# Performance work log

Hardware: AMD Instinct MI355X
Metric: run time of the kernel (lower is better)

Reference implementation:

```python
import jax, jax.numpy as jnp
import numpy as np

H, D = 8, 16
HD = H * D
SCALE0 = float(1.0 / np.sqrt(D * 1))   # degree-0 dot-product scale (order m=1)
SCALE1 = float(1.0 / np.sqrt(D * 3))   # degree-1 dot-product scale (order m=3)
SHARED = float(np.sqrt(0.5))           # shared_scale = sqrt(1/2) for DOT_PROD + SHARED
NEG = -1e9


def _split_heads_q(x):  # (b,n,HD,m) -> (b,H,n,D,m)
    b, n, _, m = x.shape
    return x.reshape(b, n, H, D, m).transpose(0, 2, 1, 3, 4)


def _split_heads_k(x):  # (b,n,N,HD,m) -> (b,H,n,N,D,m)
    b, n, N, _, m = x.shape
    return x.reshape(b, n, N, H, D, m).transpose(0, 3, 1, 2, 4, 5)


def _augment_kv(k, v, feats, W_self, null_k, null_v):
    # attend_self: VNLinear self key/value; use_null_kv: learned null tokens.
    b, n = feats.shape[:2]
    m = feats.shape[-1]
    skv = jnp.einsum('oc,bncm->bnom', W_self, feats)          # (b,n,2HD,m)
    sk, sv = jnp.split(skv, 2, axis=-2)
    sk = _split_heads_q(sk)[:, :, :, None]                     # (b,H,n,1,D,m)
    sv = _split_heads_q(sv)[:, :, :, None]
    nk = jnp.broadcast_to(null_k[None, :, None, None], (b, H, n, 1, D, m))
    nv = jnp.broadcast_to(null_v[None, :, None, None], (b, H, n, 1, D, m))
    k = jnp.concatenate([nk, sk, k], axis=3)                   # (b,H,n,2+N,D,m)
    v = jnp.concatenate([nv, sv, v], axis=3)
    return k, v


def _merge_heads(x):  # (b,H,n,D,m) -> (b,n,HD,m)
    b, _, n, _, m = x.shape
    return x.transpose(0, 2, 1, 3, 4).reshape(b, n, HD, m)


def _forward(q0, k0, v0, q1, k1, v1, feats0, feats1, edges,
             W_self_kv0, W_self_kv1, W_bias, self_bias, null_bias,
             null_k0, null_v0, null_k1, null_v1, head_weights1,
             W_out0, W_out1, neighbor_mask):
    b, n, N = edges.shape[:3]
    q0h, k0h, v0h = _split_heads_q(q0), _split_heads_k(k0), _split_heads_k(v0)
    q1h, k1h, v1h = _split_heads_q(q1), _split_heads_k(k1), _split_heads_k(v1)
    k0h, v0h = _augment_kv(k0h, v0h, feats0, W_self_kv0, null_k0, null_v0)
    k1h, v1h = _augment_kv(k1h, v1h, feats1, W_self_kv1, null_k1, null_v1)

    # pair bias for degree 0 (to_order==1); prepend null/self bias columns
    edge_bias = jnp.einsum('bnje,he->bhnj', edges, W_bias)     # (b,H,n,N)
    nb = jnp.broadcast_to(null_bias[None, :, None, None], (b, H, n, 1))
    sb = jnp.broadcast_to(self_bias[None, :, None, None], (b, H, n, 1))
    bias = jnp.concatenate([nb, sb, edge_bias], axis=-1)        # (b,H,n,2+N)

    sim0 = jnp.einsum('bhndm,bhnjdm->bhnj', q0h, k0h) * SCALE0 + bias
    w1 = jax.nn.softplus(head_weights1)                         # (1,H,1,1)
    sim1 = jnp.einsum('bhndm,bhnjdm->bhnj', q1h, k1h) * (SCALE1 * w1)

    total = (sim0 + sim1) * SHARED
    mask = jnp.concatenate(
        [jnp.ones((b, 1, n, 2), dtype=bool),                    # null + self always valid
         neighbor_mask[:, None]], axis=-1)
    total = jnp.where(mask, total, NEG)
    attn = jax.nn.softmax(total, axis=-1)                       # shared across degrees

    out0 = _merge_heads(jnp.einsum('bhnj,bhnjdm->bhndm', attn, v0h))
    out1 = _merge_heads(jnp.einsum('bhnj,bhnjdm->bhndm', attn, v1h))

    y0 = jnp.einsum('oc,bncm->bnom', W_out0, out0)              # FiberLinear deg 0
    y1 = jnp.einsum('oc,bncm->bnom', W_out1, out1)              # FiberLinear deg 1
    return y0, y1


def setup_inputs() -> dict:
    key = jax.random.key(0)
    ks = jax.random.split(key, 20)
    b, n, N, e = 1, 2048, 32, 32
    d0, d1 = 128, 64
    f = lambda k, s: jax.random.normal(k, s, dtype=jnp.float32) * 0.1
    return {
        'q0': f(ks[0], (b, n, HD, 1)), 'k0': f(ks[1], (b, n, N, HD, 1)), 'v0': f(ks[2], (b, n, N, HD, 1)),
        'q1': f(ks[3], (b, n, HD, 3)), 'k1': f(ks[4], (b, n, N, HD, 3)), 'v1': f(ks[5], (b, n, N, HD, 3)),
        'feats0': f(ks[6], (b, n, d0, 1)), 'feats1': f(ks[7], (b, n, d1, 3)),
        'edges': f(ks[8], (b, n, N, e)),
        'W_self_kv0': f(ks[9], (2 * HD, d0)), 'W_self_kv1': f(ks[10], (2 * HD, d1)),
        'W_bias': f(ks[11], (H, e)),
        'self_bias': jnp.zeros((H,), jnp.float32), 'null_bias': jnp.zeros((H,), jnp.float32),
        'null_k0': jnp.zeros((H, D, 1), jnp.float32), 'null_v0': jnp.zeros((H, D, 1), jnp.float32),
        'null_k1': jnp.zeros((H, D, 3), jnp.float32), 'null_v1': jnp.zeros((H, D, 3), jnp.float32),
        'head_weights1': jnp.full((1, H, 1, 1), float(np.log(np.e - 1.0)), jnp.float32),
        'W_out0': f(ks[12], (d0, HD)), 'W_out1': f(ks[13], (d1, HD)),
        'neighbor_mask': jax.random.uniform(ks[14], (b, n, N)) > 0.1,
    }


def reference(q0, k0, v0, q1, k1, v1, feats0, feats1, edges,
              W_self_kv0, W_self_kv1, W_bias, self_bias, null_bias,
              null_k0, null_v0, null_k1, null_v1, head_weights1,
              W_out0, W_out1, neighbor_mask):
    return _forward(q0, k0, v0, q1, k1, v1, feats0, feats1, edges,
                    W_self_kv0, W_self_kv1, W_bias, self_bias, null_bias,
                    null_k0, null_v0, null_k1, null_v1, head_weights1,
                    W_out0, W_out1, neighbor_mask)
```

## Files before the change

### kernel.cpp

```cpp
#include <hip/hip_runtime.h>

constexpr int kH  = 8;
constexpr int kD  = 16;
constexpr int kHD = 128;
constexpr int kN  = 32;
constexpr int kE  = 32;
constexpr int kD0 = 128;
constexpr int kD1 = 64;

constexpr float SCALE0   = 0.25f;
constexpr float SCALE1   = 0.14433756729740643f;
constexpr float SHARED_S = 0.70710678118654752f;
constexpr float NEGV     = -1e9f;

__global__ __launch_bounds__(256, 8) void se3_fused(
    const float* __restrict__ q0, const float* __restrict__ q1,
    const float* __restrict__ k0, const float* __restrict__ k1,
    const float* __restrict__ v0, const float* __restrict__ v1,
    const float* __restrict__ feats0, const float* __restrict__ feats1,
    const float* __restrict__ edges,
    const float* __restrict__ Wskv0, const float* __restrict__ Wskv1,
    const float* __restrict__ Wbias,
    const float* __restrict__ sbias, const float* __restrict__ nbias,
    const float* __restrict__ nk0, const float* __restrict__ nk1,
    const float* __restrict__ nv0, const float* __restrict__ nv1,
    const float* __restrict__ hw1,
    const float* __restrict__ Wout0, const float* __restrict__ Wout1,
    const int* __restrict__ nmask,
    float* __restrict__ out, int n_total)
{
  const int i = blockIdx.x;
  const int t = threadIdx.x;
  const int q4 = t & 3;
  const int qg = t >> 2;
  const int hB = qg & 7;
  const int jl = qg >> 3;

  __shared__ __align__(16) float f0s[kD0];
  __shared__ __align__(16) float f1s[kD1 * 3];
  __shared__ __align__(16) float q0s[kHD];
  __shared__ __align__(16) float q1s[kHD * 3];
  __shared__ float edg[kN * (kE + 1)];
  __shared__ float wbs[kH * kE];
  __shared__ float w1s[kH];
  __shared__ int   nmL[kN];
  __shared__ float sk0[kHD];
  __shared__ __align__(16) float sk1[kHD * 3];
  __shared__ __align__(16) float sv0[kHD];
  __shared__ __align__(16) float sv1[kHD * 3];
  __shared__ float sc[kH][36];
  __shared__ __align__(16) float o0p[2][kHD];
  __shared__ __align__(16) float o1p[2][kHD * 3];

  if (t < 32) {
    ((float4*)f0s)[t] = ((const float4*)(feats0 + (size_t)i * kD0))[t];
  } else if (t < 80) {
    ((float4*)f1s)[t - 32] = ((const float4*)(feats1 + (size_t)i * kD1 * 3))[t - 32];
  } else if (t < 112) {
    ((float4*)q0s)[t - 80] = ((const float4*)(q0 + (size_t)i * kHD))[t - 80];
  } else if (t < 208) {
    ((float4*)q1s)[t - 112] = ((const float4*)(q1 + (size_t)i * kHD * 3))[t - 112];
  }
  { float4 ev = ((const float4*)(edges + (size_t)i * kN * kE))[t];
    int j = t >> 3, e4 = (t & 7) * 4;
    float* dst = &edg[j * 33 + e4];
    dst[0] = ev.x; dst[1] = ev.y; dst[2] = ev.z; dst[3] = ev.w; }
  wbs[t] = Wbias[t];
  if (t < kN) nmL[t] = nmask[(size_t)i * kN + t];
  if (t < kH) w1s[t] = log1pf(expf(hw1[t]));
  __syncthreads();

  #pragma unroll
  for (int pass = 0; pass < 4; ++pass) {
    const int r = qg + 64 * pass;
    const float4* w0r = (const float4*)(Wskv0 + (size_t)r * kD0);
    float a0 = 0.f;
    #pragma unroll
    for (int g = 0; g < 8; ++g) {
      float4 w = w0r[q4 + 4 * g]; int c = (q4 + 4 * g) * 4;
      a0 += w.x * f0s[c] + w.y * f0s[c + 1]
          + w.z * f0s[c + 2] + w.w * f0s[c + 3];
    }
    const float4* w1r = (const float4*)(Wskv1 + (size_t)r * kD1);
    float a1[3] = {};
    #pragma unroll
    for (int g = 0; g < 4; ++g) {
      float4 w = w1r[q4 + 4 * g]; int c = (q4 + 4 * g) * 4;
      float wvv[4] = {w.x, w.y, w.z, w.w};
      #pragma unroll
      for (int k = 0; k < 4; ++k) {
        const float* fp = &f1s[(c + k) * 3];
        a1[0] += wvv[k] * fp[0];
        a1[1] += wvv[k] * fp[1];
        a1[2] += wvv[k] * fp[2];
      }
    }
    a0 += __shfl_xor(a0, 1); a0 += __shfl_xor(a0, 2);
    #pragma unroll
    for (int c = 0; c < 3; ++c) {
      a1[c] += __shfl_xor(a1[c], 1);
      a1[c] += __shfl_xor(a1[c], 2);
    }
    if (q4 == 0) {
      if (r < kHD) {
        sk0[r] = a0;
        sk1[r * 3 + 0] = a1[0]; sk1[r * 3 + 1] = a1[1]; sk1[r * 3 + 2] = a1[2];
      } else {
        const int o = r - kHD;
        sv0[o] = a0;
        sv1[o * 3 + 0] = a1[0]; sv1[o * 3 + 1] = a1[1]; sv1[o * 3 + 2] = a1[2];
      }
    }
  }
  __syncthreads();

  if (t < 16) {
    const int h = t & 7;
    const bool is_self = t >= 8;
    float s0 = 0.f, s1 = 0.f, bias;
    if (is_self) {
      #pragma unroll
      for (int d = 0; d < kD; ++d) s0 += q0s[h * kD + d] * sk0[h * kD + d];
      #pragma unroll
      for (int x = 0; x < 48; ++x) s1 += q1s[h * 48 + x] * sk1[h * 48 + x];
      bias = sbias[h];
    } else {
      #pragma unroll
      for (int d = 0; d < kD; ++d) s0 += q0s[h * kD + d] * nk0[h * kD + d];
      #pragma unroll
      for (int x = 0; x < 48; ++x) s1 += q1s[h * 48 + x] * nk1[h * 48 + x];
      bias = nbias[h];
    }
    sc[h][is_self ? 1 : 0] =
        (s0 * SCALE0 + bias + s1 * SCALE1 * w1s[h]) * SHARED_S;
  }

  {
    const float w1h = w1s[hB];
    float wbf[8];
    #pragma unroll
    for (int e = 0; e < 8; ++e) wbf[e] = wbs[hB * kE + q4 * 8 + e];
    const float4 q0f = *((const float4*)(q0s + hB * kD) + q4);
    float4 q1f[3];
    #pragma unroll
    for (int pc = 0; pc < 3; ++pc)
      q1f[pc] = *((const float4*)(q1s + hB * 48 + pc * 16) + q4);

    const float* k0base = k0 + (size_t)i * kN * kHD + hB * kD + q4 * 4;
    const float* k1base = k1 + (size_t)i * kN * kHD * 3 + hB * 48 + q4 * 4;

    float4 kv0[4];
    float4 kv1[4][3];
    #pragma unroll
    for (int pp = 0; pp < 4; ++pp) {
      const int j = pp * 8 + jl;
      kv0[pp] = *((const float4*)(k0base + (size_t)j * kHD));
      #pragma unroll
      for (int pc = 0; pc < 3; ++pc)
        kv1[pp][pc] = *((const float4*)(k1base + (size_t)j * kHD * 3 + pc * 16));
    }

    #pragma unroll
    for (int pp = 0; pp < 4; ++pp) {
      const int j = pp * 8 + jl;
      float s0 = kv0[pp].x * q0f.x + kv0[pp].y * q0f.y
               + kv0[pp].z * q0f.z + kv0[pp].w * q0f.w;
      float s1 = 0.f;
      #pragma unroll
      for (int pc = 0; pc < 3; ++pc)
        s1 += kv1[pp][pc].x * q1f[pc].x + kv1[pp][pc].y * q1f[pc].y
            + kv1[pp][pc].z * q1f[pc].z + kv1[pp][pc].w * q1f[pc].w;
      float bias = 0.f;
      #pragma unroll
      for (int e = 0; e < 8; ++e) bias += edg[j * 33 + q4 * 8 + e] * wbf[e];

      float part = s0 * SCALE0 + bias + s1 * SCALE1 * w1h;
      part += __shfl_xor(part, 1);
      part += __shfl_xor(part, 2);
      if (q4 == 0) sc[hB][2 + j] = nmL[j] ? part * SHARED_S : NEGV;
    }
  }
  __syncthreads();

  if (t < 128) {
    const int h = t >> 4, l = t & 15;
    float* rp = sc[h];
    float va = rp[2 + l], vb = rp[2 + l + 16];
    float mx = fmaxf(va, vb);
    #pragma unroll
    for (int off = 8; off > 0; off >>= 1) mx = fmaxf(mx, __shfl_xor(mx, off));
    float e0v = rp[0], e1v = rp[1];
    mx = fmaxf(mx, fmaxf(e0v, e1v));
    float ea = __expf(va - mx), eb = __expf(vb - mx);
    float sum = ea + eb;
    #pragma unroll
    for (int off = 8; off > 0; off >>= 1) sum += __shfl_xor(sum, off);
    float ee0 = __expf(e0v - mx), ee1 = __expf(e1v - mx);
    float inv = 1.f / (sum + ee0 + ee1);
    rp[2 + l] = ea * inv;
    rp[2 + l + 16] = eb * inv;
    if (l == 0) rp[0] = ee0 * inv;
    if (l == 1) rp[1] = ee1 * inv;
  }
  __syncthreads();

  {
    const int halfD = t >> 7;
    const int s = t & 127;
    float4 acc = {0.f, 0.f, 0.f, 0.f};
    if (s < 32) {
      const int h = s >> 2;
      const float* at = sc[h];
      if (halfD == 0) {
        float4 nv = ((const float4*)nv0)[s];
        float4 sv = ((const float4*)sv0)[s];
        acc.x = at[0] * nv.x + at[1] * sv.x;
        acc.y = at[0] * nv.y + at[1] * sv.y;
        acc.z = at[0] * nv.z + at[1] * sv.z;
        acc.w = at[0] * nv.w + at[1] * sv.w;
      }
      const float4* vp = (const float4*)(v0 + (size_t)i * kN * kHD) + s;
      float4 vbuf[8];
      #pragma unroll
      for (int gg = 0; gg < 2; ++gg) {
        const int g = halfD * 2 + gg;
        #pragma unroll
        for (int r = 0; r < 8; ++r) vbuf[r] = vp[(g * 8 + r) * 32];
        #pragma unroll
        for (int r = 0; r < 8; ++r) {
          float a = at[2 + g * 8 + r];
          acc.x += a * vbuf[r].x; acc.y += a * vbuf[r].y;
          acc.z += a * vbuf[r].z; acc.w += a * vbuf[r].w;
        }
      }
      ((float4*)o0p[halfD])[s] = acc;
    } else {
      const int s1 = s - 32;
      const int h = s1 / 12;
      const float* at = sc[h];
      if (halfD == 0) {
        float4 nv = ((const float4*)nv1)[s1];
        float4 sv = ((const float4*)sv1)[s1];
        acc.x = at[0] * nv.x + at[1] * sv.x;
        acc.y = at[0] * nv.y + at[1] * sv.y;
        acc.z = at[0] * nv.z + at[1] * sv.z;
        acc.w = at[0] * nv.w + at[1] * sv.w;
      }
      const float4* vp = (const float4*)(v1 + (size_t)i * kN * kHD * 3) + s1;
      float4 vbuf[8];
      #pragma unroll
      for (int gg = 0; gg < 2; ++gg) {
        const int g = halfD * 2 + gg;
        #pragma unroll
        for (int r = 0; r < 8; ++r) vbuf[r] = vp[(g * 8 + r) * 96];
        #pragma unroll
        for (int r = 0; r < 8; ++r) {
          float a = at[2 + g * 8 + r];
          acc.x += a * vbuf[r].x; acc.y += a * vbuf[r].y;
          acc.z += a * vbuf[r].z; acc.w += a * vbuf[r].w;
        }
      }
      ((float4*)o1p[halfD])[s1] = acc;
    }
  }
  __syncthreads();

  if (t < 128) {
    if (t < 32) {
      float4 a = ((float4*)o0p[0])[t], b = ((float4*)o0p[1])[t];
      a.x += b.x; a.y += b.y; a.z += b.z; a.w += b.w;
      ((float4*)o0p[0])[t] = a;
    } else {
      const int s1 = t - 32;
      float4 a = ((float4*)o1p[0])[s1], b = ((float4*)o1p[1])[s1];
      a.x += b.x; a.y += b.y; a.z += b.z; a.w += b.w;
      ((float4*)o1p[0])[s1] = a;
    }
  }
  __syncthreads();

  #pragma unroll
  for (int pass = 0; pass < 5; ++pass) {
    const int u = qg + 64 * pass;
    if (u < 128) {
      const float4* wr = (const float4*)(Wout0 + (size_t)u * kHD);
      float a = 0.f;
      #pragma unroll
      for (int g = 0; g < 8; ++g) {
        float4 w = wr[q4 + 4 * g]; int c = (q4 + 4 * g) * 4;
        a += w.x * o0p[0][c] + w.y * o0p[0][c + 1]
           + w.z * o0p[0][c + 2] + w.w * o0p[0][c + 3];
      }
      a += __shfl_xor(a, 1); a += __shfl_xor(a, 2);
      if (q4 == 0) out[(size_t)i * kHD + u] = a;
    } else {
      const int v2 = u - 128, o = v2 / 3, m = v2 - o * 3;
      const float4* wr = (const float4*)(Wout1 + (size_t)o * kHD);
      float a = 0.f;
      #pragma unroll
      for (int g = 0; g < 8; ++g) {
        float4 w = wr[q4 + 4 * g]; int c = (q4 + 4 * g) * 4;
        a += w.x * o1p[0][(c + 0) * 3 + m] + w.y * o1p[0][(c + 1) * 3 + m]
           + w.z * o1p[0][(c + 2) * 3 + m] + w.w * o1p[0][(c + 3) * 3 + m];
      }
      a += __shfl_xor(a, 1); a += __shfl_xor(a, 2);
      if (q4 == 0)
        out[(size_t)n_total * kHD + (size_t)i * 192 + v2] = a;
    }
  }
}

extern "C" void kernel_launch(void* const* d_in, const int* in_sizes, int n_in,
                              void* d_out, int out_size, void* d_ws, size_t ws_size,
                              hipStream_t stream) {
  const int n = in_sizes[0] / kHD;
  const float* q0     = (const float*)d_in[0];
  const float* k0     = (const float*)d_in[1];
  const float* v0     = (const float*)d_in[2];
  const float* q1     = (const float*)d_in[3];
  const float* k1     = (const float*)d_in[4];
  const float* v1     = (const float*)d_in[5];
  const float* feats0 = (const float*)d_in[6];
  const float* feats1 = (const float*)d_in[7];
  const float* edges  = (const float*)d_in[8];
  const float* Wskv0  = (const float*)d_in[9];
  const float* Wskv1  = (const float*)d_in[10];
  const float* Wbias  = (const float*)d_in[11];
  const float* sbias  = (const float*)d_in[12];
  const float* nbias  = (const float*)d_in[13];
  const float* nk0    = (const float*)d_in[14];
  const float* nv0    = (const float*)d_in[15];
  const float* nk1    = (const float*)d_in[16];
  const float* nv1    = (const float*)d_in[17];
  const float* hw1    = (const float*)d_in[18];
  const float* Wout0  = (const float*)d_in[19];
  const float* Wout1  = (const float*)d_in[20];
  const int*   nmask  = (const int*)d_in[21];

  se3_fused<<<n, 256, 0, stream>>>(
      q0, q1, k0, k1, v0, v1, feats0, feats1, edges,
      Wskv0, Wskv1, Wbias, sbias, nbias, nk0, nk1, nv0, nv1, hw1,
      Wout0, Wout1, nmask, (float*)d_out, n);
}
```

Before: 382.8 us.

## Shrink fused SE3 attention kernel to one 64-thread wavefront per node

Rewrites the per-node kernel to use a single 64-lane wavefront instead of 256 threads. Every phase loops over more work per thread: self-KV projection, scores, softmax, value aggregation and output projection. Edges are now read straight from global memory instead of being staged in LDS, and the split-half value accumulation with its reduction pass is removed. The intent is to cut barrier and LDS overhead and let more blocks fit per CU, at the cost of less per-block parallelism and latency hiding.

```diff
diff --git a/kernel.cpp b/kernel.cpp
--- a/kernel.cpp
+++ b/kernel.cpp
@@ -13,7 +13,7 @@
 constexpr float SHARED_S = 0.70710678118654752f;
 constexpr float NEGV     = -1e9f;
 
-__global__ __launch_bounds__(256, 8) void se3_fused(
+__global__ __launch_bounds__(64, 1) void se3_wave(
     const float* __restrict__ q0, const float* __restrict__ q1,
     const float* __restrict__ k0, const float* __restrict__ k1,
     const float* __restrict__ v0, const float* __restrict__ v1,
@@ -29,19 +29,16 @@
     const int* __restrict__ nmask,
     float* __restrict__ out, int n_total)
 {
-  const int i = blockIdx.x;
-  const int t = threadIdx.x;
+  const int i  = blockIdx.x;
+  const int t  = threadIdx.x;
   const int q4 = t & 3;
-  const int qg = t >> 2;
-  const int hB = qg & 7;
-  const int jl = qg >> 3;
+  const int qq = t >> 2;
 
   __shared__ __align__(16) float f0s[kD0];
   __shared__ __align__(16) float f1s[kD1 * 3];
   __shared__ __align__(16) float q0s[kHD];
   __shared__ __align__(16) float q1s[kHD * 3];
-  __shared__ float edg[kN * (kE + 1)];
-  __shared__ float wbs[kH * kE];
+  __shared__ __align__(16) float wbs[kH * kE];
   __shared__ float w1s[kH];
   __shared__ int   nmL[kN];
   __shared__ float sk0[kHD];
@@ -49,30 +46,23 @@
   __shared__ __align__(16) float sv0[kHD];
   __shared__ __align__(16) float sv1[kHD * 3];
   __shared__ float sc[kH][36];
-  __shared__ __align__(16) float o0p[2][kHD];
-  __shared__ __align__(16) float o1p[2][kHD * 3];
-
-  if (t < 32) {
-    ((float4*)f0s)[t] = ((const float4*)(feats0 + (size_t)i * kD0))[t];
-  } else if (t < 80) {
-    ((float4*)f1s)[t - 32] = ((const float4*)(feats1 + (size_t)i * kD1 * 3))[t - 32];
-  } else if (t < 112) {
-    ((float4*)q0s)[t - 80] = ((const float4*)(q0 + (size_t)i * kHD))[t - 80];
-  } else if (t < 208) {
-    ((float4*)q1s)[t - 112] = ((const float4*)(q1 + (size_t)i * kHD * 3))[t - 112];
-  }
-  { float4 ev = ((const float4*)(edges + (size_t)i * kN * kE))[t];
-    int j = t >> 3, e4 = (t & 7) * 4;
-    float* dst = &edg[j * 33 + e4];
-    dst[0] = ev.x; dst[1] = ev.y; dst[2] = ev.z; dst[3] = ev.w; }
-  wbs[t] = Wbias[t];
+  __shared__ __align__(16) float o0L[kHD];
+  __shared__ __align__(16) float o1L[kHD * 3];
+
+  if (t < 32) ((float4*)f0s)[t] = ((const float4*)(feats0 + (size_t)i * kD0))[t];
+  if (t < 48) ((float4*)f1s)[t] = ((const float4*)(feats1 + (size_t)i * kD1 * 3))[t];
+  if (t < 32) ((float4*)q0s)[t] = ((const float4*)(q0 + (size_t)i * kHD))[t];
+  #pragma unroll
+  for (int u = t; u < 96; u += 64)
+    ((float4*)q1s)[u] = ((const float4*)(q1 + (size_t)i * kHD * 3))[u];
+  ((float4*)wbs)[t] = ((const float4*)Wbias)[t];
   if (t < kN) nmL[t] = nmask[(size_t)i * kN + t];
   if (t < kH) w1s[t] = log1pf(expf(hw1[t]));
   __syncthreads();
 
-  #pragma unroll
-  for (int pass = 0; pass < 4; ++pass) {
-    const int r = qg + 64 * pass;
+  #pragma unroll 4
+  for (int pass = 0; pass < 16; ++pass) {
+    const int r = qq + 16 * pass;
     const float4* w0r = (const float4*)(Wskv0 + (size_t)r * kD0);
     float a0 = 0.f;
     #pragma unroll
@@ -136,94 +126,90 @@
   }
 
   {
-    const float w1h = w1s[hB];
+    const int h  = qq & 7;
+    const int jh = qq >> 3;
+    const float w1h = w1s[h];
     float wbf[8];
     #pragma unroll
-    for (int e = 0; e < 8; ++e) wbf[e] = wbs[hB * kE + q4 * 8 + e];
-    const float4 q0f = *((const float4*)(q0s + hB * kD) + q4);
+    for (int e = 0; e < 8; ++e) wbf[e] = wbs[h * kE + q4 * 8 + e];
+    const float4 q0f = *((const float4*)(q0s + h * kD) + q4);
     float4 q1f[3];
     #pragma unroll
     for (int pc = 0; pc < 3; ++pc)
-      q1f[pc] = *((const float4*)(q1s + hB * 48 + pc * 16) + q4);
-
-    const float* k0base = k0 + (size_t)i * kN * kHD + hB * kD + q4 * 4;
-    const float* k1base = k1 + (size_t)i * kN * kHD * 3 + hB * 48 + q4 * 4;
-
-    float4 kv0[4];
-    float4 kv1[4][3];
-    #pragma unroll
-    for (int pp = 0; pp < 4; ++pp) {
-      const int j = pp * 8 + jl;
-      kv0[pp] = *((const float4*)(k0base + (size_t)j * kHD));
-      #pragma unroll
-      for (int pc = 0; pc < 3; ++pc)
-        kv1[pp][pc] = *((const float4*)(k1base + (size_t)j * kHD * 3 + pc * 16));
-    }
-
-    #pragma unroll
-    for (int pp = 0; pp < 4; ++pp) {
-      const int j = pp * 8 + jl;
-      float s0 = kv0[pp].x * q0f.x + kv0[pp].y * q0f.y
-               + kv0[pp].z * q0f.z + kv0[pp].w * q0f.w;
-      float s1 = 0.f;
-      #pragma unroll
-      for (int pc = 0; pc < 3; ++pc)
-        s1 += kv1[pp][pc].x * q1f[pc].x + kv1[pp][pc].y * q1f[pc].y
-            + kv1[pp][pc].z * q1f[pc].z + kv1[pp][pc].w * q1f[pc].w;
-      float bias = 0.f;
-      #pragma unroll
-      for (int e = 0; e < 8; ++e) bias += edg[j * 33 + q4 * 8 + e] * wbf[e];
-
-      float part = s0 * SCALE0 + bias + s1 * SCALE1 * w1h;
+      q1f[pc] = *((const float4*)(q1s + h * 48 + pc * 16) + q4);
+
+    const float* k0base = k0 + (size_t)i * kN * kHD + h * kD + q4 * 4;
+    const float* k1base = k1 + (size_t)i * kN * kHD * 3 + h * 48 + q4 * 4;
+    const float* ebase  = edges + (size_t)i * kN * kE + q4 * 8;
+
+    #pragma unroll 4
+    for (int jj = 0; jj < 16; ++jj) {
+      const int j = jh * 16 + jj;
+      float4 ka = *((const float4*)(k0base + (size_t)j * kHD));
+      float4 kb0 = *((const float4*)(k1base + (size_t)j * kHD * 3));
+      float4 kb1 = *((const float4*)(k1base + (size_t)j * kHD * 3 + 16));
+      float4 kb2 = *((const float4*)(k1base + (size_t)j * kHD * 3 + 32));
+      float4 e0 = ((const float4*)(ebase + (size_t)j * kE))[0];
+      float4 e1 = ((const float4*)(ebase + (size_t)j * kE))[1];
+
+      float s0 = ka.x * q0f.x + ka.y * q0f.y + ka.z * q0f.z + ka.w * q0f.w;
+      float s1 = kb0.x * q1f[0].x + kb0.y * q1f[0].y
+               + kb0.z * q1f[0].z + kb0.w * q1f[0].w
+               + kb1.x * q1f[1].x + kb1.y * q1f[1].y
+               + kb1.z * q1f[1].z + kb1.w * q1f[1].w
+               + kb2.x * q1f[2].x + kb2.y * q1f[2].y
+               + kb2.z * q1f[2].z + kb2.w * q1f[2].w;
+      float bias = e0.x * wbf[0] + e0.y * wbf[1] + e0.z * wbf[2] + e0.w * wbf[3]
+                 + e1.x * wbf[4] + e1.y * wbf[5] + e1.z * wbf[6] + e1.w * wbf[7];
+
+      float part = s0 * SCALE0 + s1 * SCALE1 * w1h + bias;
       part += __shfl_xor(part, 1);
       part += __shfl_xor(part, 2);
-      if (q4 == 0) sc[hB][2 + j] = nmL[j] ? part * SHARED_S : NEGV;
-    }
-  }
-  __syncthreads();
-
-  if (t < 128) {
-    const int h = t >> 4, l = t & 15;
+      if (q4 == 0) sc[h][2 + j] = nmL[j] ? part * SHARED_S : NEGV;
+    }
+  }
+  __syncthreads();
+
+  {
+    const int h = t >> 3, l = t & 7;
     float* rp = sc[h];
-    float va = rp[2 + l], vb = rp[2 + l + 16];
-    float mx = fmaxf(va, vb);
-    #pragma unroll
-    for (int off = 8; off > 0; off >>= 1) mx = fmaxf(mx, __shfl_xor(mx, off));
+    float va = rp[2 + l], vb = rp[2 + l + 8], vc = rp[2 + l + 16], vd = rp[2 + l + 24];
+    float mx = fmaxf(fmaxf(va, vb), fmaxf(vc, vd));
+    #pragma unroll
+    for (int off = 4; off > 0; off >>= 1) mx = fmaxf(mx, __shfl_xor(mx, off));
     float e0v = rp[0], e1v = rp[1];
     mx = fmaxf(mx, fmaxf(e0v, e1v));
     float ea = __expf(va - mx), eb = __expf(vb - mx);
-    float sum = ea + eb;
-    #pragma unroll
-    for (int off = 8; off > 0; off >>= 1) sum += __shfl_xor(sum, off);
+    float ec = __expf(vc - mx), ed = __expf(vd - mx);
+    float sum = (ea + eb) + (ec + ed);
+    #pragma unroll
+    for (int off = 4; off > 0; off >>= 1) sum += __shfl_xor(sum, off);
     float ee0 = __expf(e0v - mx), ee1 = __expf(e1v - mx);
     float inv = 1.f / (sum + ee0 + ee1);
     rp[2 + l] = ea * inv;
-    rp[2 + l + 16] = eb * inv;
+    rp[2 + l + 8] = eb * inv;
+    rp[2 + l + 16] = ec * inv;
+    rp[2 + l + 24] = ed * inv;
     if (l == 0) rp[0] = ee0 * inv;
     if (l == 1) rp[1] = ee1 * inv;
   }
   __syncthreads();
 
   {
-    const int halfD = t >> 7;
-    const int s = t & 127;
-    float4 acc = {0.f, 0.f, 0.f, 0.f};
-    if (s < 32) {
-      const int h = s >> 2;
+    if (t < 32) {
+      const int s = t, h = s >> 2;
       const float* at = sc[h];
-      if (halfD == 0) {
-        float4 nv = ((const float4*)nv0)[s];
-        float4 sv = ((const float4*)sv0)[s];
-        acc.x = at[0] * nv.x + at[1] * sv.x;
-        acc.y = at[0] * nv.y + at[1] * sv.y;
-        acc.z = at[0] * nv.z + at[1] * sv.z;
-        acc.w = at[0] * nv.w + at[1] * sv.w;
-      }
+      float4 nv = ((const float4*)nv0)[s];
+      float4 sv = ((const float4*)sv0)[s];
+      float4 acc;
+      acc.x = at[0] * nv.x + at[1] * sv.x;
+      acc.y = at[0] * nv.y + at[1] * sv.y;
+      acc.z = at[0] * nv.z + at[1] * sv.z;
+      acc.w = at[0] * nv.w + at[1] * sv.w;
       const float4* vp = (const float4*)(v0 + (size_t)i * kN * kHD) + s;
       float4 vbuf[8];
       #pragma unroll
-      for (int gg = 0; gg < 2; ++gg) {
-        const int g = halfD * 2 + gg;
+      for (int g = 0; g < 4; ++g) {
         #pragma unroll
         for (int r = 0; r < 8; ++r) vbuf[r] = vp[(g * 8 + r) * 32];
         #pragma unroll
@@ -233,24 +219,21 @@
           acc.z += a * vbuf[r].z; acc.w += a * vbuf[r].w;
         }
       }
-      ((float4*)o0p[halfD])[s] = acc;
+      ((float4*)o0L)[s] = acc;
     } else {
-      const int s1 = s - 32;
-      const int h = s1 / 12;
+      const int s1 = t - 32, h = s1 / 12;
       const float* at = sc[h];
-      if (halfD == 0) {
-        float4 nv = ((const float4*)nv1)[s1];
-        float4 sv = ((const float4*)sv1)[s1];
-        acc.x = at[0] * nv.x + at[1] * sv.x;
-        acc.y = at[0] * nv.y + at[1] * sv.y;
-        acc.z = at[0] * nv.z + at[1] * sv.z;
-        acc.w = at[0] * nv.w + at[1] * sv.w;
-      }
+      float4 nv = ((const float4*)nv1)[s1];
+      float4 sv = ((const float4*)sv1)[s1];
+      float4 acc;
+      acc.x = at[0] * nv.x + at[1] * sv.x;
+      acc.y = at[0] * nv.y + at[1] * sv.y;
+      acc.z = at[0] * nv.z + at[1] * sv.z;
+      acc.w = at[0] * nv.w + at[1] * sv.w;
       const float4* vp = (const float4*)(v1 + (size_t)i * kN * kHD * 3) + s1;
       float4 vbuf[8];
       #pragma unroll
-      for (int gg = 0; gg < 2; ++gg) {
-        const int g = halfD * 2 + gg;
+      for (int g = 0; g < 4; ++g) {
         #pragma unroll
         for (int r = 0; r < 8; ++r) vbuf[r] = vp[(g * 8 + r) * 96];
         #pragma unroll
@@ -260,36 +243,47 @@
           acc.z += a * vbuf[r].z; acc.w += a * vbuf[r].w;
         }
       }
-      ((float4*)o1p[halfD])[s1] = acc;
-    }
-  }
-  __syncthreads();
-
-  if (t < 128) {
-    if (t < 32) {
-      float4 a = ((float4*)o0p[0])[t], b = ((float4*)o0p[1])[t];
-      a.x += b.x; a.y += b.y; a.z += b.z; a.w += b.w;
-      ((float4*)o0p[0])[t] = a;
-    } else {
-      const int s1 = t - 32;
-      float4 a = ((float4*)o1p[0])[s1], b = ((float4*)o1p[1])[s1];
-      a.x += b.x; a.y += b.y; a.z += b.z; a.w += b.w;
-      ((float4*)o1p[0])[s1] = a;
-    }
-  }
-  __syncthreads();
-
-  #pragma unroll
-  for (int pass = 0; pass < 5; ++pass) {
-    const int u = qg + 64 * pass;
+      ((float4*)o1L)[s1] = acc;
+    }
+    {
+      const int s1 = t + 32, h = s1 / 12;
+      const float* at = sc[h];
+      float4 nv = ((const float4*)nv1)[s1];
+      float4 sv = ((const float4*)sv1)[s1];
+      float4 acc;
+      acc.x = at[0] * nv.x + at[1] * sv.x;
+      acc.y = at[0] * nv.y + at[1] * sv.y;
+      acc.z = at[0] * nv.z + at[1] * sv.z;
+      acc.w = at[0] * nv.w + at[1] * sv.w;
+      const float4* vp = (const float4*)(v1 + (size_t)i * kN * kHD * 3) + s1;
+      float4 vbuf[8];
+      #pragma unroll
+      for (int g = 0; g < 4; ++g) {
+        #pragma unroll
+        for (int r = 0; r < 8; ++r) vbuf[r] = vp[(g * 8 + r) * 96];
+        #pragma unroll
+        for (int r = 0; r < 8; ++r) {
+          float a = at[2 + g * 8 + r];
+          acc.x += a * vbuf[r].x; acc.y += a * vbuf[r].y;
+          acc.z += a * vbuf[r].z; acc.w += a * vbuf[r].w;
+        }
+      }
+      ((float4*)o1L)[s1] = acc;
+    }
+  }
+  __syncthreads();
+
+  #pragma unroll 2
+  for (int p = 0; p < 20; ++p) {
+    const int u = 16 * p + qq;
     if (u < 128) {
       const float4* wr = (const float4*)(Wout0 + (size_t)u * kHD);
       float a = 0.f;
       #pragma unroll
       for (int g = 0; g < 8; ++g) {
         float4 w = wr[q4 + 4 * g]; int c = (q4 + 4 * g) * 4;
-        a += w.x * o0p[0][c] + w.y * o0p[0][c + 1]
-           + w.z * o0p[0][c + 2] + w.w * o0p[0][c + 3];
+        a += w.x * o0L[c] + w.y * o0L[c + 1]
+           + w.z * o0L[c + 2] + w.w * o0L[c + 3];
       }
       a += __shfl_xor(a, 1); a += __shfl_xor(a, 2);
       if (q4 == 0) out[(size_t)i * kHD + u] = a;
@@ -300,8 +294,8 @@
       #pragma unroll
       for (int g = 0; g < 8; ++g) {
         float4 w = wr[q4 + 4 * g]; int c = (q4 + 4 * g) * 4;
-        a += w.x * o1p[0][(c + 0) * 3 + m] + w.y * o1p[0][(c + 1) * 3 + m]
-           + w.z * o1p[0][(c + 2) * 3 + m] + w.w * o1p[0][(c + 3) * 3 + m];
+        a += w.x * o1L[(c + 0) * 3 + m] + w.y * o1L[(c + 1) * 3 + m]
+           + w.z * o1L[(c + 2) * 3 + m] + w.w * o1L[(c + 3) * 3 + m];
       }
       a += __shfl_xor(a, 1); a += __shfl_xor(a, 2);
       if (q4 == 0)
@@ -337,7 +331,7 @@
   const float* Wout1  = (const float*)d_in[20];
   const int*   nmask  = (const int*)d_in[21];
 
-  se3_fused<<<n, 256, 0, stream>>>(
+  se3_wave<<<n, 64, 0, stream>>>(
       q0, q1, k0, k1, v0, v1, feats0, feats1, edges,
       Wskv0, Wskv1, Wbias, sbias, nbias, nk0, nk1, nv0, nv1, hw1,
       Wout0, Wout1, nmask, (float*)d_out, n);
```

New measurement: 370.4 us. 3.2% less time.
